# Performance work log

Hardware: AMD Instinct MI355X
Metric: run time of the kernel (lower is better)

Reference implementation:

```python
import jax, jax.numpy as jnp
import numpy as np

H = 24  # num_heads
EPS = 1e-6

def _ln(x):
    m = jnp.mean(x, -1, keepdims=True)
    v = jnp.mean((x - m) ** 2, -1, keepdims=True)
    return (x - m) * jax.lax.rsqrt(v + EPS)

def _rms(x, w):
    return x * jax.lax.rsqrt(jnp.mean(x * x, -1, keepdims=True) + EPS) * w

def _rope(x, pe):
    # x: [B,H,L,Dh], pe: [1,1,L,Dh//2,2,2]
    b, h, l, d = x.shape
    xr = x.reshape(b, h, l, d // 2, 1, 2)
    out = pe[..., 0] * xr[..., 0] + pe[..., 1] * xr[..., 1]  # [B,H,L,Dh//2,2]
    return out.reshape(b, h, l, d)

def _mod6(vec, w, b):
    out = jnp.dot(jax.nn.silu(vec), w) + b  # [B, 6*D]
    return jnp.split(out[:, None, :], 6, axis=-1)  # six [B,1,D]

def _stream_qkv(x, shift, scale, qkv_w, qkv_b, qn, kn):
    xm = (1 + scale) * _ln(x) + shift
    qkv = jnp.dot(xm, qkv_w) + qkv_b  # [B,L,3D]
    B, L, _ = qkv.shape
    qkv = qkv.reshape(B, L, 3, H, -1).transpose(2, 0, 3, 1, 4)  # [3,B,H,L,Dh]
    q, k, v = qkv[0], qkv[1], qkv[2]
    return _rms(q, qn), _rms(k, kn), v

def _forward(img, txt, vec, pe,
             img_mod_w, img_mod_b, img_qkv_w, img_qkv_b, img_qnorm, img_knorm,
             img_proj_w, img_proj_b, img_mlp_w1, img_mlp_b1, img_mlp_w2, img_mlp_b2,
             txt_mod_w, txt_mod_b, txt_qkv_w, txt_qkv_b, txt_qnorm, txt_knorm,
             txt_proj_w, txt_proj_b, txt_mlp_w1, txt_mlp_b1, txt_mlp_w2, txt_mlp_b2):
    i_sh1, i_sc1, i_g1, i_sh2, i_sc2, i_g2 = _mod6(vec, img_mod_w, img_mod_b)
    t_sh1, t_sc1, t_g1, t_sh2, t_sc2, t_g2 = _mod6(vec, txt_mod_w, txt_mod_b)
    iq, ik, iv = _stream_qkv(img, i_sh1, i_sc1, img_qkv_w, img_qkv_b, img_qnorm, img_knorm)
    tq, tk, tv = _stream_qkv(txt, t_sh1, t_sc1, txt_qkv_w, txt_qkv_b, txt_qnorm, txt_knorm)
    q = jnp.concatenate([tq, iq], axis=2)
    k = jnp.concatenate([tk, ik], axis=2)
    v = jnp.concatenate([tv, iv], axis=2)
    q = _rope(q, pe)
    k = _rope(k, pe)
    dh = q.shape[-1]
    scores = jnp.einsum('bhqd,bhkd->bhqk', q, k) / jnp.sqrt(jnp.asarray(dh, q.dtype))
    probs = jax.nn.softmax(scores, axis=-1)
    attn = jnp.einsum('bhqk,bhkd->bhqd', probs, v)
    B, _, L, _ = attn.shape
    attn = attn.transpose(0, 2, 1, 3).reshape(B, L, -1)  # [B,L,H*Dh]
    Lt = txt.shape[1]
    t_att, i_att = attn[:, :Lt], attn[:, Lt:]
    img = img + i_g1 * (jnp.dot(i_att, img_proj_w) + img_proj_b)
    img_in2 = (1 + i_sc2) * _ln(img) + i_sh2
    img = img + i_g2 * (jnp.dot(jax.nn.gelu(jnp.dot(img_in2, img_mlp_w1) + img_mlp_b1, approximate=True), img_mlp_w2) + img_mlp_b2)
    txt = txt + t_g1 * (jnp.dot(t_att, txt_proj_w) + txt_proj_b)
    txt_in2 = (1 + t_sc2) * _ln(txt) + t_sh2
    txt = txt + t_g2 * (jnp.dot(jax.nn.gelu(jnp.dot(txt_in2, txt_mlp_w1) + txt_mlp_b1, approximate=True), txt_mlp_w2) + txt_mlp_b2)
    return img, txt

def setup_inputs() -> dict:
    key = jax.random.key(0)
    ks = jax.random.split(key, 24)
    D, Dh, M = 3072, 128, 12288
    B, Li, Lt = 1, 1024, 256
    L = Li + Lt
    s = 0.02
    inp = {
        'img': jax.random.normal(ks[0], (B, Li, D), jnp.float32),
        'txt': jax.random.normal(ks[1], (B, Lt, D), jnp.float32),
        'vec': jax.random.normal(ks[2], (B, D), jnp.float32),
        'pe': jax.random.normal(ks[3], (1, 1, L, Dh // 2, 2, 2), jnp.float32),
        'img_mod_w': jax.random.normal(ks[4], (D, 6 * D), jnp.float32) * s,
        'img_mod_b': jnp.zeros((6 * D,), jnp.float32),
        'img_qkv_w': jax.random.normal(ks[5], (D, 3 * D), jnp.float32) * s,
        'img_qkv_b': jnp.zeros((3 * D,), jnp.float32),
        'img_qnorm': jnp.ones((Dh,), jnp.float32),
        'img_knorm': jnp.ones((Dh,), jnp.float32),
        'img_proj_w': jax.random.normal(ks[6], (D, D), jnp.float32) * s,
        'img_proj_b': jnp.zeros((D,), jnp.float32),
        'img_mlp_w1': jax.random.normal(ks[7], (D, M), jnp.float32) * s,
        'img_mlp_b1': jnp.zeros((M,), jnp.float32),
        'img_mlp_w2': jax.random.normal(ks[8], (M, D), jnp.float32) * s,
        'img_mlp_b2': jnp.zeros((D,), jnp.float32),
        'txt_mod_w': jax.random.normal(ks[9], (D, 6 * D), jnp.float32) * s,
        'txt_mod_b': jnp.zeros((6 * D,), jnp.float32),
        'txt_qkv_w': jax.random.normal(ks[10], (D, 3 * D), jnp.float32) * s,
        'txt_qkv_b': jnp.zeros((3 * D,), jnp.float32),
        'txt_qnorm': jnp.ones((Dh,), jnp.float32),
        'txt_knorm': jnp.ones((Dh,), jnp.float32),
        'txt_proj_w': jax.random.normal(ks[11], (D, D), jnp.float32) * s,
        'txt_proj_b': jnp.zeros((D,), jnp.float32),
        'txt_mlp_w1': jax.random.normal(ks[12], (D, M), jnp.float32) * s,
        'txt_mlp_b1': jnp.zeros((M,), jnp.float32),
        'txt_mlp_w2': jax.random.normal(ks[13], (M, D), jnp.float32) * s,
        'txt_mlp_b2': jnp.zeros((D,), jnp.float32),
    }
    return inp

def reference(img, txt, vec, pe,
              img_mod_w, img_mod_b, img_qkv_w, img_qkv_b, img_qnorm, img_knorm,
              img_proj_w, img_proj_b, img_mlp_w1, img_mlp_b1, img_mlp_w2, img_mlp_b2,
              txt_mod_w, txt_mod_b, txt_qkv_w, txt_qkv_b, txt_qnorm, txt_knorm,
              txt_proj_w, txt_proj_b, txt_mlp_w1, txt_mlp_b1, txt_mlp_w2, txt_mlp_b2):
    return _forward(img, txt, vec, pe,
                    img_mod_w, img_mod_b, img_qkv_w, img_qkv_b, img_qnorm, img_knorm,
                    img_proj_w, img_proj_b, img_mlp_w1, img_mlp_b1, img_mlp_w2, img_mlp_b2,
                    txt_mod_w, txt_mod_b, txt_qkv_w, txt_qkv_b, txt_qnorm, txt_knorm,
                    txt_proj_w, txt_proj_b, txt_mlp_w1, txt_mlp_b1, txt_mlp_w2, txt_mlp_b2)
```

## Files before the change

### kernel.cpp

```cpp
#include <hip/hip_runtime.h>
#include <hip/hip_bf16.h>
#include <math.h>

#define D_MODEL 3072
#define N_HEADS 24
#define DH 128
#define L_TXT 256
#define L_IMG 1024
#define L_ALL 1280
#define N_QKV 9216
#define N_MLP 12288
#define MOD_N 18432

typedef __attribute__((ext_vector_type(4))) float f32x4;
typedef __attribute__((ext_vector_type(8))) short bf16x8;

static __device__ __forceinline__ unsigned short f2bf(float f) {
  __hip_bfloat16 h = __float2bfloat16(f);
  union { __hip_bfloat16 h; unsigned short u; } v; v.h = h;
  return v.u;
}
static __device__ __forceinline__ unsigned pack2(float a, float b) {
  return (unsigned)f2bf(a) | ((unsigned)f2bf(b) << 16);
}

__global__ void silu_kernel(const float* __restrict__ vec, float* __restrict__ s) {
  int i = blockIdx.x * 256 + threadIdx.x;
  if (i < D_MODEL) { float x = vec[i]; s[i] = x / (1.f + expf(-x)); }
}

__global__ __launch_bounds__(256) void mod_gemv_partial(
    const float* __restrict__ s, const float* __restrict__ w_img,
    const float* __restrict__ w_txt, float* __restrict__ part) {
  int col4 = blockIdx.x * 256 + threadIdx.x;
  int kb = blockIdx.y;
  const float4* w4 = (const float4*)(blockIdx.z == 0 ? w_img : w_txt);
  float4 acc = {0.f, 0.f, 0.f, 0.f};
  int k0 = kb * 192;
  #pragma unroll 4
  for (int j = 0; j < 192; ++j) {
    float sv = s[k0 + j];
    float4 wv = w4[(size_t)(k0 + j) * 4608 + col4];
    acc.x = fmaf(sv, wv.x, acc.x);
    acc.y = fmaf(sv, wv.y, acc.y);
    acc.z = fmaf(sv, wv.z, acc.z);
    acc.w = fmaf(sv, wv.w, acc.w);
  }
  ((float4*)part)[(size_t)(blockIdx.z * 16 + kb) * 4608 + col4] = acc;
}

__global__ void mod_reduce(const float* __restrict__ part,
                           const float* __restrict__ b_img,
                           const float* __restrict__ b_txt,
                           float* __restrict__ modv) {
  int i = blockIdx.x * 256 + threadIdx.x;
  int st = i / MOD_N, col = i - st * MOD_N;
  float a = (st == 0) ? b_img[col] : b_txt[col];
  #pragma unroll
  for (int p = 0; p < 16; ++p) a += part[(st * 16 + p) * MOD_N + col];
  modv[i] = a;
}

__global__ __launch_bounds__(256) void ln_mod_kernel(
    const float* __restrict__ x, unsigned short* __restrict__ xm,
    const float* __restrict__ modv, int sh_off, int sc_off) {
  int row = blockIdx.x, t = threadIdx.x;
  int lane = t & 63, wid = t >> 6;
  const float4* xr = (const float4*)(x + (size_t)row * D_MODEL);
  float4 a = xr[t], b = xr[t + 256], c = xr[t + 512];
  float s = a.x + a.y + a.z + a.w + b.x + b.y + b.z + b.w + c.x + c.y + c.z + c.w;
  float q = a.x * a.x + a.y * a.y + a.z * a.z + a.w * a.w
          + b.x * b.x + b.y * b.y + b.z * b.z + b.w * b.w
          + c.x * c.x + c.y * c.y + c.z * c.z + c.w * c.w;
  #pragma unroll
  for (int m = 1; m < 64; m <<= 1) { s += __shfl_xor(s, m); q += __shfl_xor(q, m); }
  __shared__ float red[8];
  if (lane == 0) { red[wid] = s; red[4 + wid] = q; }
  __syncthreads();
  s = red[0] + red[1] + red[2] + red[3];
  q = red[4] + red[5] + red[6] + red[7];
  float mean = s * (1.f / 3072.f);
  float var = q * (1.f / 3072.f) - mean * mean;
  float inv = 1.f / sqrtf(var + 1e-6f);
  const float4* shp = (const float4*)(modv + sh_off);
  const float4* scp = (const float4*)(modv + sc_off);
  uint2* outp = (uint2*)(xm + (size_t)row * D_MODEL);
  float4 vals[3] = {a, b, c};
  #pragma unroll
  for (int j = 0; j < 3; ++j) {
    float4 sh = shp[t + j * 256], sc = scp[t + j * 256];
    float4 v = vals[j];
    float y0 = (v.x - mean) * inv * (1.f + sc.x) + sh.x;
    float y1 = (v.y - mean) * inv * (1.f + sc.y) + sh.y;
    float y2 = (v.z - mean) * inv * (1.f + sc.z) + sh.z;
    float y3 = (v.w - mean) * inv * (1.f + sc.w) + sh.w;
    uint2 o; o.x = pack2(y0, y1); o.y = pack2(y2, y3);
    outp[t + j * 256] = o;
  }
}

template <int EPI>
__global__ __launch_bounds__(512, 2) void gemm15_kernel(
    const unsigned short* __restrict__ A0, const float* __restrict__ W0,
    const float* __restrict__ b0, float* __restrict__ oF0,
    float* __restrict__ oF0b, unsigned short* __restrict__ oB0,
    const unsigned short* __restrict__ A1, const float* __restrict__ W1,
    const float* __restrict__ b1, float* __restrict__ oF1,
    float* __restrict__ oF1b, unsigned short* __restrict__ oB1,
    int mi, int mt, int N, int Ktot, int Kper) {
  __shared__ __align__(16) unsigned short Alds[4][8192];
  __shared__ __align__(16) unsigned short Wlds[2][4128];

  const int MT = mi + mt;
  const int q8 = gridDim.x >> 3;
  int orig = (blockIdx.x & 7) * q8 + (blockIdx.x >> 3);
  const int per_k = (N >> 7) * MT;
  const int kz = orig / per_k; orig -= kz * per_k;
  const int ntile = orig / MT;
  const int mrem = orig - ntile * MT;

  const unsigned short* A; const float* W; const float* bias;
  float* outF; unsigned short* outB; int brow;
  if (mrem < mi) {
    A = A0; W = W0; bias = b0; outF = kz ? oF0b : oF0; outB = oB0; brow = mrem * 256;
  } else {
    A = A1; W = W1; bias = b1; outF = kz ? oF1b : oF1; outB = oB1; brow = (mrem - mi) * 256;
  }
  const int bcol = ntile * 128;
  const int k0base = kz * Kper;

  const int tid = threadIdx.x, lane = tid & 63, wid = tid >> 6;
  const int lm = lane & 15, lk = lane >> 4;
  const int wr = (wid >> 1) * 64, wc = (wid & 1) * 64;
  const int aslot = lk ^ ((lm >> 1) & 3);

  const int arw = lane >> 2;
  const int achk = (lane & 3) ^ ((lane >> 3) & 3);
  const int koct0 = tid >> 7;
  const int ncol = tid & 127;
  const size_t Ns = (size_t)N;
  const float* wgp = W + bcol + ncol;

  f32x4 acc[4][4] = {};
  float w0[8], w1[8], w2[8];
  const int nt = Kper >> 5;

  auto STAGE_A = [&](int buf, int t) {
    const int kc = k0base + t * 32 + achk * 8;
    #pragma unroll
    for (int u = 0; u < 2; ++u) {
      const int j = wid * 2 + u;
      const unsigned short* g = A + (size_t)(brow + j * 16 + arw) * Ktot + kc;
      __builtin_amdgcn_global_load_lds(g, &Alds[buf][j * 512], 16, 0, 0);
    }
  };
  auto LOADW = [&](float (&w)[8], int t) {
    const size_t kb = (size_t)(k0base + t * 32 + koct0 * 8) * Ns;
    #pragma unroll
    for (int i = 0; i < 8; ++i)
      w[i] = wgp[kb + (size_t)i * Ns];
  };
  auto PACKW = [&](unsigned short* wbuf, float (&w)[8]) {
    uint4 p;
    p.x = pack2(w[0], w[1]); p.y = pack2(w[2], w[3]);
    p.z = pack2(w[4], w[5]); p.w = pack2(w[6], w[7]);
    *(uint4*)&wbuf[koct0 * 1032 + ncol * 8] = p;
  };
  auto MFMA16 = [&](const unsigned short* wbuf, int abuf) {
    bf16x8 bfr[4], af[4];
    #pragma unroll
    for (int nf = 0; nf < 4; ++nf)
      bfr[nf] = *(const bf16x8*)&wbuf[lk * 1032 + (wc + nf * 16 + lm) * 8];
    #pragma unroll
    for (int mf = 0; mf < 4; ++mf) {
      const int row = wr + mf * 16 + lm;
      af[mf] = *(const bf16x8*)&Alds[abuf][row * 32 + aslot * 8];
    }
    __builtin_amdgcn_s_setprio(1);
    #pragma unroll
    for (int mf = 0; mf < 4; ++mf)
      #pragma unroll
      for (int nf = 0; nf < 4; ++nf)
        acc[mf][nf] = __builtin_amdgcn_mfma_f32_16x16x32_bf16(af[mf], bfr[nf], acc[mf][nf], 0, 0, 0);
    __builtin_amdgcn_s_setprio(0);
  };

  auto PHASE = [&](int i, float (&wload)[8], float (&wpack)[8]) {
    if (i + 2 < nt) STAGE_A((i + 2) & 3, i + 2);
    if (i + 3 < nt) LOADW(wload, i + 3);
    if (i + 1 < nt) PACKW(&Wlds[(i + 1) & 1][0], wpack);
    MFMA16(&Wlds[i & 1][0], i & 3);
    __builtin_amdgcn_sched_barrier(0);
    asm volatile("s_waitcnt lgkmcnt(0)");
    if (i + 3 < nt) asm volatile("s_waitcnt vmcnt(18)");
    else            asm volatile("s_waitcnt vmcnt(0)");
    __builtin_amdgcn_s_barrier();
    __builtin_amdgcn_sched_barrier(0);
  };

  STAGE_A(0, 0);
  LOADW(w0, 0);
  STAGE_A(1, 1);
  LOADW(w1, 1);
  LOADW(w2, 2);
  PACKW(&Wlds[0][0], w0);
  __builtin_amdgcn_sched_barrier(0);
  asm volatile("s_waitcnt lgkmcnt(0)");
  asm volatile("s_waitcnt vmcnt(18)");
  __builtin_amdgcn_s_barrier();
  __builtin_amdgcn_sched_barrier(0);

  for (int i = 0; i < nt; i += 3) {
    PHASE(i + 0, w0, w1);
    PHASE(i + 1, w1, w2);
    PHASE(i + 2, w2, w0);
  }

  #pragma unroll
  for (int nf = 0; nf < 4; ++nf) {
    int c = bcol + wc + nf * 16 + lm;
    float bv = (EPI == 3) ? 0.f : bias[c];
    #pragma unroll
    for (int mf = 0; mf < 4; ++mf) {
      int r0 = brow + wr + mf * 16 + lk * 4;
      #pragma unroll
      for (int rg = 0; rg < 4; ++rg) {
        float v = acc[mf][nf][rg] + bv;
        size_t idx = (size_t)(r0 + rg) * N + c;
        if (EPI == 0) {
          outF[idx] = v;
        } else if (EPI == 1) {
          float g = 0.5f * v * (1.f + tanhf(0.7978845608028654f * (v + 0.044715f * v * v * v)));
          outB[idx] = f2bf(g);
        } else {
          outF[idx] = v;
        }
      }
    }
  }
}

__global__ __launch_bounds__(256) void split_reduce_kernel(
    const float* __restrict__ s0, const float* __restrict__ s1,
    const float* __restrict__ res, const float* __restrict__ bias,
    const float* __restrict__ gate, float* __restrict__ out,
    int n4, int ncol4) {
  int i = blockIdx.x * 256 + threadIdx.x;
  if (i >= n4) return;
  int c4 = i % ncol4;
  float4 a = ((const float4*)s0)[i];
  float4 b = ((const float4*)s1)[i];
  float4 bv = ((const float4*)bias)[c4];
  float4 gv = ((const float4*)gate)[c4];
  float4 rv = ((const float4*)res)[i];
  float4 o;
  o.x = rv.x + gv.x * (a.x + b.x + bv.x);
  o.y = rv.y + gv.y * (a.y + b.y + bv.y);
  o.z = rv.z + gv.z * (a.z + b.z + bv.z);
  o.w = rv.w + gv.w * (a.w + b.w + bv.w);
  ((float4*)out)[i] = o;
}

__global__ __launch_bounds__(256) void rms_rope_kernel(
    const float* __restrict__ qkv_img, const float* __restrict__ qkv_txt,
    const float* __restrict__ img_qn, const float* __restrict__ img_kn,
    const float* __restrict__ txt_qn, const float* __restrict__ txt_kn,
    const float* __restrict__ pe, unsigned short* __restrict__ qa,
    unsigned short* __restrict__ ka, unsigned short* __restrict__ va) {
  int l = blockIdx.x * 4 + (threadIdx.x >> 6);
  int h = blockIdx.y;
  int t = threadIdx.x & 63;
  const float* base; const float* qn; const float* kn;
  if (l < L_TXT) { base = qkv_txt + (size_t)l * N_QKV; qn = txt_qn; kn = txt_kn; }
  else { base = qkv_img + (size_t)(l - L_TXT) * N_QKV; qn = img_qn; kn = img_kn; }
  int d0 = 2 * t;
  float q0 = base[h * DH + d0], q1 = base[h * DH + d0 + 1];
  float k0 = base[D_MODEL + h * DH + d0], k1 = base[D_MODEL + h * DH + d0 + 1];
  float v0 = base[2 * D_MODEL + h * DH + d0], v1 = base[2 * D_MODEL + h * DH + d0 + 1];
  float sq = q0 * q0 + q1 * q1, sk = k0 * k0 + k1 * k1;
  #pragma unroll
  for (int m = 1; m < 64; m <<= 1) { sq += __shfl_xor(sq, m); sk += __shfl_xor(sk, m); }
  float rq = 1.f / sqrtf(sq * (1.f / 128.f) + 1e-6f);
  float rk = 1.f / sqrtf(sk * (1.f / 128.f) + 1e-6f);
  q0 *= rq * qn[d0]; q1 *= rq * qn[d0 + 1];
  k0 *= rk * kn[d0]; k1 *= rk * kn[d0 + 1];
  const float* p = pe + ((size_t)l * 64 + t) * 4;
  float p00 = p[0], p01 = p[1], p10 = p[2], p11 = p[3];
  const float sc = 0.08838834764831845f;
  float Q0 = (p00 * q0 + p01 * q1) * sc;
  float Q1 = (p10 * q0 + p11 * q1) * sc;
  float K0 = p00 * k0 + p01 * k1;
  float K1 = p10 * k0 + p11 * k1;
  size_t o = ((size_t)h * L_ALL + l) * 64 + t;
  ((unsigned*)qa)[o] = pack2(Q0, Q1);
  ((unsigned*)ka)[o] = pack2(K0, K1);
  ((unsigned*)va)[o] = pack2(v0, v1);
}

static __device__ __forceinline__ void stage_v8(unsigned short* vp, int n0, uint4 v) {
  vp[(n0 + 0) * 8] = (unsigned short)v.x; vp[(n0 + 1) * 8] = (unsigned short)(v.x >> 16);
  vp[(n0 + 2) * 8] = (unsigned short)v.y; vp[(n0 + 3) * 8] = (unsigned short)(v.y >> 16);
  vp[(n0 + 4) * 8] = (unsigned short)v.z; vp[(n0 + 5) * 8] = (unsigned short)(v.z >> 16);
  vp[(n0 + 6) * 8] = (unsigned short)v.w; vp[(n0 + 7) * 8] = (unsigned short)(v.w >> 16);
}

__global__ __launch_bounds__(256) void attn_kernel(
    const unsigned short* __restrict__ qa, const unsigned short* __restrict__ ka,
    const unsigned short* __restrict__ va, unsigned short* __restrict__ out) {
  __shared__ __align__(16) unsigned short Ks[64 * 136];
  __shared__ __align__(16) unsigned short Vs[16 * 128 * 8];
  __shared__ __align__(16) unsigned short Ps[4][16 * 72];
  int h = blockIdx.y, qt = blockIdx.x;
  int tid = threadIdx.x, lane = tid & 63, wid = tid >> 6;
  int lm = lane & 15, lk = lane >> 4;
  const unsigned short* qh = qa + (size_t)h * L_ALL * DH;
  const unsigned short* kh = ka + (size_t)h * L_ALL * DH;
  const unsigned short* vh = va + (size_t)h * L_ALL * DH;

  int qrow = qt * 64 + wid * 16 + lm;
  bf16x8 qf[4];
  #pragma unroll
  for (int kk = 0; kk < 4; ++kk)
    qf[kk] = *(const bf16x8*)(qh + (size_t)qrow * DH + kk * 32 + lk * 8);

  float m_run[4] = {-INFINITY, -INFINITY, -INFINITY, -INFINITY};
  float s_run[4] = {0.f, 0.f, 0.f, 0.f};
  f32x4 o[8] = {};

  int sr = tid >> 2, sc = (tid & 3) * 32;

  for (int kt = 0; kt < L_ALL / 64; ++kt) {
    const uint4* kg = (const uint4*)(kh + (size_t)(kt * 64 + sr) * DH + sc);
    uint4 kv0 = kg[0], kv1 = kg[1], kv2 = kg[2], kv3 = kg[3];
    const uint4* vg = (const uint4*)(vh + (size_t)(kt * 64 + sr) * DH + sc);
    uint4 vv0 = vg[0], vv1 = vg[1], vv2 = vg[2], vv3 = vg[3];
    __syncthreads();
    uint4* kd = (uint4*)(&Ks[sr * 136 + sc]);
    kd[0] = kv0; kd[1] = kv1; kd[2] = kv2; kd[3] = kv3;
    {
      unsigned short* vp = &Vs[(sr >> 3) * 1024 + (sr & 7)];
      stage_v8(vp, sc, vv0); stage_v8(vp, sc + 8, vv1);
      stage_v8(vp, sc + 16, vv2); stage_v8(vp, sc + 24, vv3);
    }
    __syncthreads();

    f32x4 S[4] = {};
    #pragma unroll
    for (int kk = 0; kk < 4; ++kk)
      #pragma unroll
      for (int nf = 0; nf < 4; ++nf) {
        bf16x8 bv = *(const bf16x8*)(&Ks[(nf * 16 + lm) * 136 + kk * 32 + lk * 8]);
        S[nf] = __builtin_amdgcn_mfma_f32_16x16x32_bf16(qf[kk], bv, S[nf], 0, 0, 0);
      }

    float corr[4];
    #pragma unroll
    for (int r = 0; r < 4; ++r) {
      float mx = fmaxf(fmaxf(S[0][r], S[1][r]), fmaxf(S[2][r], S[3][r]));
      mx = fmaxf(mx, __shfl_xor(mx, 1));
      mx = fmaxf(mx, __shfl_xor(mx, 2));
      mx = fmaxf(mx, __shfl_xor(mx, 4));
      mx = fmaxf(mx, __shfl_xor(mx, 8));
      float mn = fmaxf(m_run[r], mx);
      corr[r] = expf(m_run[r] - mn);
      m_run[r] = mn;
    }
    float rs[4] = {0.f, 0.f, 0.f, 0.f};
    float pv[4][4];
    #pragma unroll
    for (int nf = 0; nf < 4; ++nf)
      #pragma unroll
      for (int r = 0; r < 4; ++r) {
        pv[nf][r] = expf(S[nf][r] - m_run[r]);
        rs[r] += pv[nf][r];
      }
    #pragma unroll
    for (int nf = 0; nf < 4; ++nf)
      #pragma unroll
      for (int r = 0; r < 4; ++r)
        Ps[wid][(lk * 4 + r) * 72 + nf * 16 + lm] = f2bf(pv[nf][r]);
    #pragma unroll
    for (int r = 0; r < 4; ++r) {
      rs[r] += __shfl_xor(rs[r], 1);
      rs[r] += __shfl_xor(rs[r], 2);
      rs[r] += __shfl_xor(rs[r], 4);
      rs[r] += __shfl_xor(rs[r], 8);
      s_run[r] = s_run[r] * corr[r] + rs[r];
    }
    #pragma unroll
    for (int nf = 0; nf < 8; ++nf)
      #pragma unroll
      for (int r = 0; r < 4; ++r)
        o[nf][r] *= corr[r];

    #pragma unroll
    for (int kk2 = 0; kk2 < 2; ++kk2) {
      bf16x8 pa = *(const bf16x8*)(&Ps[wid][lm * 72 + kk2 * 32 + lk * 8]);
      #pragma unroll
      for (int nf = 0; nf < 8; ++nf) {
        bf16x8 vb = *(const bf16x8*)(&Vs[((kk2 * 4 + lk) * 128 + nf * 16 + lm) * 8]);
        o[nf] = __builtin_amdgcn_mfma_f32_16x16x32_bf16(pa, vb, o[nf], 0, 0, 0);
      }
    }
  }

  float inv[4];
  #pragma unroll
  for (int r = 0; r < 4; ++r) inv[r] = 1.f / s_run[r];
  #pragma unroll
  for (int nf = 0; nf < 8; ++nf)
    #pragma unroll
    for (int r = 0; r < 4; ++r) {
      int row = qt * 64 + wid * 16 + lk * 4 + r;
      int col = h * DH + nf * 16 + lm;
      out[(size_t)row * D_MODEL + col] = f2bf(o[nf][r] * inv[r]);
    }
}

extern "C" void kernel_launch(void* const* d_in, const int* in_sizes, int n_in,
                              void* d_out, int out_size, void* d_ws, size_t ws_size,
                              hipStream_t stream) {
  const float* img = (const float*)d_in[0];
  const float* txt = (const float*)d_in[1];
  const float* vec = (const float*)d_in[2];
  const float* pe = (const float*)d_in[3];
  const float* img_mod_w = (const float*)d_in[4];
  const float* img_mod_b = (const float*)d_in[5];
  const float* img_qkv_w = (const float*)d_in[6];
  const float* img_qkv_b = (const float*)d_in[7];
  const float* img_qnorm = (const float*)d_in[8];
  const float* img_knorm = (const float*)d_in[9];
  const float* img_proj_w = (const float*)d_in[10];
  const float* img_proj_b = (const float*)d_in[11];
  const float* img_mlp_w1 = (const float*)d_in[12];
  const float* img_mlp_b1 = (const float*)d_in[13];
  const float* img_mlp_w2 = (const float*)d_in[14];
  const float* img_mlp_b2 = (const float*)d_in[15];
  const float* txt_mod_w = (const float*)d_in[16];
  const float* txt_mod_b = (const float*)d_in[17];
  const float* txt_qkv_w = (const float*)d_in[18];
  const float* txt_qkv_b = (const float*)d_in[19];
  const float* txt_qnorm = (const float*)d_in[20];
  const float* txt_knorm = (const float*)d_in[21];
  const float* txt_proj_w = (const float*)d_in[22];
  const float* txt_proj_b = (const float*)d_in[23];
  const float* txt_mlp_w1 = (const float*)d_in[24];
  const float* txt_mlp_b1 = (const float*)d_in[25];
  const float* txt_mlp_w2 = (const float*)d_in[26];
  const float* txt_mlp_b2 = (const float*)d_in[27];

  char* wsb = (char*)d_ws;
  float* silu_s = (float*)(wsb + 0);
  float* part = (float*)(wsb + 16384);
  float* modv = (float*)(wsb + 2375680);
  unsigned short* xm_img = (unsigned short*)(wsb + 2523136);
  unsigned short* xm_txt = xm_img + (size_t)L_IMG * D_MODEL;
  float* qkv_img = (float*)(wsb + 10387456);
  float* qkv_txt = qkv_img + (size_t)L_IMG * N_QKV;
  unsigned short* qa = (unsigned short*)(wsb + 57573376);
  unsigned short* ka = (unsigned short*)(wsb + 65437696);
  unsigned short* va = (unsigned short*)(wsb + 73302016);
  unsigned short* attn = xm_img;
  float* img2 = (float*)(wsb + 10387456);
  float* txt2 = img2 + (size_t)L_IMG * D_MODEL;
  float* pslab = (float*)(wsb + 26116096);
  float* pslab1 = pslab + (size_t)L_ALL * D_MODEL;
  unsigned short* h_img = (unsigned short*)(wsb + 26116096);
  unsigned short* h_txt = h_img + (size_t)L_IMG * N_MLP;
  unsigned short* xm2_img = qa;
  unsigned short* xm2_txt = xm2_img + (size_t)L_IMG * D_MODEL;
  float* m2slab1 = (float*)(wsb + 57573376);
  float* out_img = (float*)d_out;
  float* out_txt = out_img + (size_t)L_IMG * D_MODEL;
  float* mod_img = modv;
  float* mod_txt = modv + MOD_N;

  silu_kernel<<<12, 256, 0, stream>>>(vec, silu_s);
  mod_gemv_partial<<<dim3(18, 16, 2), 256, 0, stream>>>(silu_s, img_mod_w, txt_mod_w, part);
  mod_reduce<<<144, 256, 0, stream>>>(part, img_mod_b, txt_mod_b, modv);
  ln_mod_kernel<<<L_IMG, 256, 0, stream>>>(img, xm_img, mod_img, 0, 3072);
  ln_mod_kernel<<<L_TXT, 256, 0, stream>>>(txt, xm_txt, mod_txt, 0, 3072);

  gemm15_kernel<0><<<360, 512, 0, stream>>>(
      xm_img, img_qkv_w, img_qkv_b, qkv_img, qkv_img, nullptr,
      xm_txt, txt_qkv_w, txt_qkv_b, qkv_txt, qkv_txt, nullptr,
      4, 1, N_QKV, D_MODEL, D_MODEL);

  rms_rope_kernel<<<dim3(L_ALL / 4, N_HEADS), 256, 0, stream>>>(qkv_img, qkv_txt, img_qnorm, img_knorm, txt_qnorm, txt_knorm, pe, qa, ka, va);
  attn_kernel<<<dim3(L_ALL / 64, N_HEADS), 256, 0, stream>>>(qa, ka, va, attn);

  gemm15_kernel<3><<<240, 512, 0, stream>>>(
      attn + (size_t)L_TXT * D_MODEL, img_proj_w, img_proj_b, pslab, pslab1, nullptr,
      attn, txt_proj_w, txt_proj_b, pslab + (size_t)L_IMG * D_MODEL, pslab1 + (size_t)L_IMG * D_MODEL, nullptr,
      4, 1, D_MODEL, D_MODEL, 1536);
  split_reduce_kernel<<<3072, 256, 0, stream>>>(
      pslab, pslab1, img, img_proj_b, mod_img + 6144, img2, L_IMG * 768, 768);
  split_reduce_kernel<<<768, 256, 0, stream>>>(
      pslab + (size_t)L_IMG * D_MODEL, pslab1 + (size_t)L_IMG * D_MODEL, txt, txt_proj_b, mod_txt + 6144, txt2, L_TXT * 768, 768);

  ln_mod_kernel<<<L_IMG, 256, 0, stream>>>(img2, xm2_img, mod_img, 9216, 12288);
  ln_mod_kernel<<<L_TXT, 256, 0, stream>>>(txt2, xm2_txt, mod_txt, 9216, 12288);

  gemm15_kernel<1><<<480, 512, 0, stream>>>(
      xm2_img, img_mlp_w1, img_mlp_b1, nullptr, nullptr, h_img,
      xm2_txt, txt_mlp_w1, txt_mlp_b1, nullptr, nullptr, h_txt,
      4, 1, N_MLP, D_MODEL, D_MODEL);

  gemm15_kernel<3><<<240, 512, 0, stream>>>(
      h_img, img_mlp_w2, img_mlp_b2, out_img, m2slab1, nullptr,
      h_txt, txt_mlp_w2, txt_mlp_b2, out_txt, m2slab1 + (size_t)L_IMG * D_MODEL, nullptr,
      4, 1, D_MODEL, N_MLP, 6144);
  split_reduce_kernel<<<3072, 256, 0, stream>>>(
      out_img, m2slab1, img2, img_mlp_b2, mod_img + 15360, out_img, L_IMG * 768, 768);
  split_reduce_kernel<<<768, 256, 0, stream>>>(
      out_txt, m2slab1 + (size_t)L_IMG * D_MODEL, txt2, txt_mlp_b2, mod_txt + 15360, out_txt, L_TXT * 768, 768);
}
```

Measured before the change: 1.020 ms.

## Pre-convert weights to bf16 and drop split-K with fused residual epilogue

Adds a separate kernel that converts fp32 weights into a packed bf16 k-octet layout in workspace, done in halves to fit the buffer. The GEMM then stages weights straight into LDS with async global-to-LDS loads instead of loading and packing fp32 in registers. The GEMM also moves to 256-thread blocks with 128-row tiles, removes split-K, and fuses the residual-plus-gate epilogue, which eliminates the split_reduce kernels and their partial-sum traffic. In exchange, every call pays an extra pass that reads the fp32 weights and writes bf16 copies, and each GEMM now covers only half of N per launch.

```diff
diff --git a/kernel.cpp b/kernel.cpp
--- a/kernel.cpp
+++ b/kernel.cpp
@@ -99,35 +99,55 @@
   }
 }
 
+__global__ __launch_bounds__(256) void wconv_kernel(
+    const float* __restrict__ src0, const float* __restrict__ src1,
+    unsigned short* __restrict__ dst, int Nsrc, int Ndst, int ncol0,
+    size_t strm) {
+  const float* src = blockIdx.z ? src1 : src0;
+  unsigned short* d = dst + blockIdx.z * strm;
+  int n = blockIdx.x * 256 + threadIdx.x;
+  int ko = blockIdx.y;
+  const float* s = src + (size_t)(ko * 8) * Nsrc + ncol0 + n;
+  float v[8];
+  #pragma unroll
+  for (int i = 0; i < 8; ++i) v[i] = s[(size_t)i * Nsrc];
+  uint4 p;
+  p.x = pack2(v[0], v[1]); p.y = pack2(v[2], v[3]);
+  p.z = pack2(v[4], v[5]); p.w = pack2(v[6], v[7]);
+  *(uint4*)&d[((size_t)ko * Ndst + n) * 8] = p;
+}
+
 template <int EPI>
-__global__ __launch_bounds__(512, 2) void gemm15_kernel(
-    const unsigned short* __restrict__ A0, const float* __restrict__ W0,
+__global__ __launch_bounds__(256, 3) void gemm16_kernel(
+    const unsigned short* __restrict__ A0, const unsigned short* __restrict__ Wh0,
     const float* __restrict__ b0, float* __restrict__ oF0,
-    float* __restrict__ oF0b, unsigned short* __restrict__ oB0,
-    const unsigned short* __restrict__ A1, const float* __restrict__ W1,
+    unsigned short* __restrict__ oB0, const float* __restrict__ res0,
+    const float* __restrict__ gate0,
+    const unsigned short* __restrict__ A1, const unsigned short* __restrict__ Wh1,
     const float* __restrict__ b1, float* __restrict__ oF1,
-    float* __restrict__ oF1b, unsigned short* __restrict__ oB1,
-    int mi, int mt, int N, int Ktot, int Kper) {
-  __shared__ __align__(16) unsigned short Alds[4][8192];
+    unsigned short* __restrict__ oB1, const float* __restrict__ res1,
+    const float* __restrict__ gate1,
+    int mi, int mt, int Nw, int Nout, int K) {
+  __shared__ __align__(16) unsigned short Alds[4][4096];
   __shared__ __align__(16) unsigned short Wlds[2][4128];
 
   const int MT = mi + mt;
   const int q8 = gridDim.x >> 3;
   int orig = (blockIdx.x & 7) * q8 + (blockIdx.x >> 3);
-  const int per_k = (N >> 7) * MT;
-  const int kz = orig / per_k; orig -= kz * per_k;
   const int ntile = orig / MT;
   const int mrem = orig - ntile * MT;
 
-  const unsigned short* A; const float* W; const float* bias;
-  float* outF; unsigned short* outB; int brow;
+  const unsigned short* A; const unsigned short* Wh; const float* bias;
+  float* outF; unsigned short* outB; const float* res; const float* gate;
+  int brow;
   if (mrem < mi) {
-    A = A0; W = W0; bias = b0; outF = kz ? oF0b : oF0; outB = oB0; brow = mrem * 256;
+    A = A0; Wh = Wh0; bias = b0; outF = oF0; outB = oB0; res = res0; gate = gate0;
+    brow = mrem * 128;
   } else {
-    A = A1; W = W1; bias = b1; outF = kz ? oF1b : oF1; outB = oB1; brow = (mrem - mi) * 256;
+    A = A1; Wh = Wh1; bias = b1; outF = oF1; outB = oB1; res = res1; gate = gate1;
+    brow = (mrem - mi) * 128;
   }
   const int bcol = ntile * 128;
-  const int k0base = kz * Kper;
 
   const int tid = threadIdx.x, lane = tid & 63, wid = tid >> 6;
   const int lm = lane & 15, lk = lane >> 4;
@@ -136,41 +156,32 @@
 
   const int arw = lane >> 2;
   const int achk = (lane & 3) ^ ((lane >> 3) & 3);
-  const int koct0 = tid >> 7;
-  const int ncol = tid & 127;
-  const size_t Ns = (size_t)N;
-  const float* wgp = W + bcol + ncol;
+  const size_t Nws = (size_t)Nw;
 
   f32x4 acc[4][4] = {};
-  float w0[8], w1[8], w2[8];
-  const int nt = Kper >> 5;
+  const int nt = K >> 5;
 
   auto STAGE_A = [&](int buf, int t) {
-    const int kc = k0base + t * 32 + achk * 8;
+    const int kc = t * 32 + achk * 8;
     #pragma unroll
     for (int u = 0; u < 2; ++u) {
       const int j = wid * 2 + u;
-      const unsigned short* g = A + (size_t)(brow + j * 16 + arw) * Ktot + kc;
+      const unsigned short* g = A + (size_t)(brow + j * 16 + arw) * K + kc;
       __builtin_amdgcn_global_load_lds(g, &Alds[buf][j * 512], 16, 0, 0);
     }
   };
-  auto LOADW = [&](float (&w)[8], int t) {
-    const size_t kb = (size_t)(k0base + t * 32 + koct0 * 8) * Ns;
-    #pragma unroll
-    for (int i = 0; i < 8; ++i)
-      w[i] = wgp[kb + (size_t)i * Ns];
+  auto STAGE_W = [&](int buf, int t) {
+    const size_t base = ((size_t)(t * 4 + wid) * Nws + bcol) * 8;
+    const unsigned short* g0 = Wh + base + (size_t)lane * 8;
+    const unsigned short* g1 = g0 + 512;
+    __builtin_amdgcn_global_load_lds(g0, &Wlds[buf][wid * 1032], 16, 0, 0);
+    __builtin_amdgcn_global_load_lds(g1, &Wlds[buf][wid * 1032 + 512], 16, 0, 0);
   };
-  auto PACKW = [&](unsigned short* wbuf, float (&w)[8]) {
-    uint4 p;
-    p.x = pack2(w[0], w[1]); p.y = pack2(w[2], w[3]);
-    p.z = pack2(w[4], w[5]); p.w = pack2(w[6], w[7]);
-    *(uint4*)&wbuf[koct0 * 1032 + ncol * 8] = p;
-  };
-  auto MFMA16 = [&](const unsigned short* wbuf, int abuf) {
+  auto MFMA16 = [&](int wbuf, int abuf) {
     bf16x8 bfr[4], af[4];
     #pragma unroll
     for (int nf = 0; nf < 4; ++nf)
-      bfr[nf] = *(const bf16x8*)&wbuf[lk * 1032 + (wc + nf * 16 + lm) * 8];
+      bfr[nf] = *(const bf16x8*)&Wlds[wbuf][lk * 1032 + (wc + nf * 16 + lm) * 8];
     #pragma unroll
     for (int mf = 0; mf < 4; ++mf) {
       const int row = wr + mf * 16 + lm;
@@ -185,80 +196,50 @@
     __builtin_amdgcn_s_setprio(0);
   };
 
-  auto PHASE = [&](int i, float (&wload)[8], float (&wpack)[8]) {
+  STAGE_A(0, 0);
+  STAGE_W(0, 0);
+  STAGE_A(1, 1);
+  __builtin_amdgcn_sched_barrier(0);
+  asm volatile("s_waitcnt vmcnt(2)");
+  __builtin_amdgcn_s_barrier();
+  __builtin_amdgcn_sched_barrier(0);
+
+  for (int i = 0; i < nt; ++i) {
+    if (i + 1 < nt) STAGE_W((i + 1) & 1, i + 1);
     if (i + 2 < nt) STAGE_A((i + 2) & 3, i + 2);
-    if (i + 3 < nt) LOADW(wload, i + 3);
-    if (i + 1 < nt) PACKW(&Wlds[(i + 1) & 1][0], wpack);
-    MFMA16(&Wlds[i & 1][0], i & 3);
+    MFMA16(i & 1, i & 3);
     __builtin_amdgcn_sched_barrier(0);
     asm volatile("s_waitcnt lgkmcnt(0)");
-    if (i + 3 < nt) asm volatile("s_waitcnt vmcnt(18)");
+    if (i + 2 < nt) asm volatile("s_waitcnt vmcnt(2)");
     else            asm volatile("s_waitcnt vmcnt(0)");
     __builtin_amdgcn_s_barrier();
     __builtin_amdgcn_sched_barrier(0);
-  };
-
-  STAGE_A(0, 0);
-  LOADW(w0, 0);
-  STAGE_A(1, 1);
-  LOADW(w1, 1);
-  LOADW(w2, 2);
-  PACKW(&Wlds[0][0], w0);
-  __builtin_amdgcn_sched_barrier(0);
-  asm volatile("s_waitcnt lgkmcnt(0)");
-  asm volatile("s_waitcnt vmcnt(18)");
-  __builtin_amdgcn_s_barrier();
-  __builtin_amdgcn_sched_barrier(0);
-
-  for (int i = 0; i < nt; i += 3) {
-    PHASE(i + 0, w0, w1);
-    PHASE(i + 1, w1, w2);
-    PHASE(i + 2, w2, w0);
   }
 
   #pragma unroll
   for (int nf = 0; nf < 4; ++nf) {
     int c = bcol + wc + nf * 16 + lm;
-    float bv = (EPI == 3) ? 0.f : bias[c];
+    float bv = bias[c];
+    float gv = 0.f;
+    if (EPI == 2) gv = gate[c];
     #pragma unroll
     for (int mf = 0; mf < 4; ++mf) {
       int r0 = brow + wr + mf * 16 + lk * 4;
       #pragma unroll
       for (int rg = 0; rg < 4; ++rg) {
         float v = acc[mf][nf][rg] + bv;
-        size_t idx = (size_t)(r0 + rg) * N + c;
+        size_t idx = (size_t)(r0 + rg) * Nout + c;
         if (EPI == 0) {
           outF[idx] = v;
         } else if (EPI == 1) {
           float g = 0.5f * v * (1.f + tanhf(0.7978845608028654f * (v + 0.044715f * v * v * v)));
           outB[idx] = f2bf(g);
         } else {
-          outF[idx] = v;
+          outF[idx] = res[idx] + gv * v;
         }
       }
     }
   }
-}
-
-__global__ __launch_bounds__(256) void split_reduce_kernel(
-    const float* __restrict__ s0, const float* __restrict__ s1,
-    const float* __restrict__ res, const float* __restrict__ bias,
-    const float* __restrict__ gate, float* __restrict__ out,
-    int n4, int ncol4) {
-  int i = blockIdx.x * 256 + threadIdx.x;
-  if (i >= n4) return;
-  int c4 = i % ncol4;
-  float4 a = ((const float4*)s0)[i];
-  float4 b = ((const float4*)s1)[i];
-  float4 bv = ((const float4*)bias)[c4];
-  float4 gv = ((const float4*)gate)[c4];
-  float4 rv = ((const float4*)res)[i];
-  float4 o;
-  o.x = rv.x + gv.x * (a.x + b.x + bv.x);
-  o.y = rv.y + gv.y * (a.y + b.y + bv.y);
-  o.z = rv.z + gv.z * (a.z + b.z + bv.z);
-  o.w = rv.w + gv.w * (a.w + b.w + bv.w);
-  ((float4*)out)[i] = o;
 }
 
 __global__ __launch_bounds__(256) void rms_rope_kernel(
@@ -461,15 +442,13 @@
   unsigned short* ka = (unsigned short*)(wsb + 65437696);
   unsigned short* va = (unsigned short*)(wsb + 73302016);
   unsigned short* attn = xm_img;
+  unsigned short* xm2_img = xm_img;
+  unsigned short* xm2_txt = xm2_img + (size_t)L_IMG * D_MODEL;
   float* img2 = (float*)(wsb + 10387456);
   float* txt2 = img2 + (size_t)L_IMG * D_MODEL;
-  float* pslab = (float*)(wsb + 26116096);
-  float* pslab1 = pslab + (size_t)L_ALL * D_MODEL;
   unsigned short* h_img = (unsigned short*)(wsb + 26116096);
   unsigned short* h_txt = h_img + (size_t)L_IMG * N_MLP;
-  unsigned short* xm2_img = qa;
-  unsigned short* xm2_txt = xm2_img + (size_t)L_IMG * D_MODEL;
-  float* m2slab1 = (float*)(wsb + 57573376);
+  unsigned short* Wc = (unsigned short*)(wsb + 57573376);
   float* out_img = (float*)d_out;
   float* out_txt = out_img + (size_t)L_IMG * D_MODEL;
   float* mod_img = modv;
@@ -481,37 +460,58 @@
   ln_mod_kernel<<<L_IMG, 256, 0, stream>>>(img, xm_img, mod_img, 0, 3072);
   ln_mod_kernel<<<L_TXT, 256, 0, stream>>>(txt, xm_txt, mod_txt, 0, 3072);
 
-  gemm15_kernel<0><<<360, 512, 0, stream>>>(
-      xm_img, img_qkv_w, img_qkv_b, qkv_img, qkv_img, nullptr,
-      xm_txt, txt_qkv_w, txt_qkv_b, qkv_txt, qkv_txt, nullptr,
-      4, 1, N_QKV, D_MODEL, D_MODEL);
+  {
+    const size_t strm = (size_t)D_MODEL * 4608;
+    for (int hlf = 0; hlf < 2; ++hlf) {
+      int nc = hlf * 4608;
+      wconv_kernel<<<dim3(18, 384, 2), 256, 0, stream>>>(
+          img_qkv_w, txt_qkv_w, Wc, N_QKV, 4608, nc, strm);
+      gemm16_kernel<0><<<360, 256, 0, stream>>>(
+          xm_img, Wc, img_qkv_b + nc, qkv_img + nc, nullptr, nullptr, nullptr,
+          xm_txt, Wc + strm, txt_qkv_b + nc, qkv_txt + nc, nullptr, nullptr, nullptr,
+          8, 2, 4608, N_QKV, D_MODEL);
+    }
+  }
 
   rms_rope_kernel<<<dim3(L_ALL / 4, N_HEADS), 256, 0, stream>>>(qkv_img, qkv_txt, img_qnorm, img_knorm, txt_qnorm, txt_knorm, pe, qa, ka, va);
   attn_kernel<<<dim3(L_ALL / 64, N_HEADS), 256, 0, stream>>>(qa, ka, va, attn);
 
-  gemm15_kernel<3><<<240, 512, 0, stream>>>(
-      attn + (size_t)L_TXT * D_MODEL, img_proj_w, img_proj_b, pslab, pslab1, nullptr,
-      attn, txt_proj_w, txt_proj_b, pslab + (size_t)L_IMG * D_MODEL, pslab1 + (size_t)L_IMG * D_MODEL, nullptr,
-      4, 1, D_MODEL, D_MODEL, 1536);
-  split_reduce_kernel<<<3072, 256, 0, stream>>>(
-      pslab, pslab1, img, img_proj_b, mod_img + 6144, img2, L_IMG * 768, 768);
-  split_reduce_kernel<<<768, 256, 0, stream>>>(
-      pslab + (size_t)L_IMG * D_MODEL, pslab1 + (size_t)L_IMG * D_MODEL, txt, txt_proj_b, mod_txt + 6144, txt2, L_TXT * 768, 768);
+  {
+    const size_t strm = (size_t)D_MODEL * D_MODEL;
+    wconv_kernel<<<dim3(12, 384, 2), 256, 0, stream>>>(
+        img_proj_w, txt_proj_w, Wc, D_MODEL, D_MODEL, 0, strm);
+    gemm16_kernel<2><<<240, 256, 0, stream>>>(
+        attn + (size_t)L_TXT * D_MODEL, Wc, img_proj_b, img2, nullptr, img, mod_img + 6144,
+        attn, Wc + strm, txt_proj_b, txt2, nullptr, txt, mod_txt + 6144,
+        8, 2, D_MODEL, D_MODEL, D_MODEL);
+  }
 
   ln_mod_kernel<<<L_IMG, 256, 0, stream>>>(img2, xm2_img, mod_img, 9216, 12288);
   ln_mod_kernel<<<L_TXT, 256, 0, stream>>>(txt2, xm2_txt, mod_txt, 9216, 12288);
 
-  gemm15_kernel<1><<<480, 512, 0, stream>>>(
-      xm2_img, img_mlp_w1, img_mlp_b1, nullptr, nullptr, h_img,
-      xm2_txt, txt_mlp_w1, txt_mlp_b1, nullptr, nullptr, h_txt,
-      4, 1, N_MLP, D_MODEL, D_MODEL);
-
-  gemm15_kernel<3><<<240, 512, 0, stream>>>(
-      h_img, img_mlp_w2, img_mlp_b2, out_img, m2slab1, nullptr,
-      h_txt, txt_mlp_w2, txt_mlp_b2, out_txt, m2slab1 + (size_t)L_IMG * D_MODEL, nullptr,
-      4, 1, D_MODEL, N_MLP, 6144);
-  split_reduce_kernel<<<3072, 256, 0, stream>>>(
-      out_img, m2slab1, img2, img_mlp_b2, mod_img + 15360, out_img, L_IMG * 768, 768);
-  split_reduce_kernel<<<768, 256, 0, stream>>>(
-      out_txt, m2slab1 + (size_t)L_IMG * D_MODEL, txt2, txt_mlp_b2, mod_txt + 15360, out_txt, L_TXT * 768, 768);
-}
+  {
+    const size_t strm = (size_t)D_MODEL * 6144;
+    for (int hlf = 0; hlf < 2; ++hlf) {
+      int nc = hlf * 6144;
+      wconv_kernel<<<dim3(24, 384, 2), 256, 0, stream>>>(
+          img_mlp_w1, txt_mlp_w1, Wc, N_MLP, 6144, nc, strm);
+      gemm16_kernel<1><<<480, 256, 0, stream>>>(
+          xm2_img, Wc, img_mlp_b1 + nc, nullptr, h_img + nc, nullptr, nullptr,
+          xm2_txt, Wc + strm, txt_mlp_b1 + nc, nullptr, h_txt + nc, nullptr, nullptr,
+          8, 2, 6144, N_MLP, D_MODEL);
+    }
+  }
+
+  {
+    const size_t strm = (size_t)N_MLP * 1536;
+    for (int hlf = 0; hlf < 2; ++hlf) {
+      int nc = hlf * 1536;
+      wconv_kernel<<<dim3(6, 1536, 2), 256, 0, stream>>>(
+          img_mlp_w2, txt_mlp_w2, Wc, D_MODEL, 1536, nc, strm);
+      gemm16_kernel<2><<<120, 256, 0, stream>>>(
+          h_img, Wc, img_mlp_b2 + nc, out_img + nc, nullptr, img2 + nc, mod_img + 15360 + nc,
+          h_txt, Wc + strm, txt_mlp_b2 + nc, out_txt + nc, nullptr, txt2 + nc, mod_txt + 15360 + nc,
+          8, 2, 1536, D_MODEL, N_MLP);
+    }
+  }
+}
```

Result: slower. 1.369 ms (+34.2%).
